# Optimization experiments

Hardware: AMD Instinct MI355X
Metric: run time of the kernel (lower is better)

Reference implementation:

```python
import jax, jax.numpy as jnp
import numpy as np

B, S, HID = 2, 2048, 2048
H, KV, D = 32, 4, 128
G = H // KV
EPS = 1e-6
SCALE = D ** -0.5
ROPE_THETA = 1000000.0


def setup_inputs() -> dict:
    key = jax.random.key(0)
    ks = jax.random.split(key, 6)
    hidden_states = jax.random.normal(ks[0], (B, S, HID), jnp.float32)
    # real RoPE tables (position_embeddings passed into forward)
    inv_freq = 1.0 / (ROPE_THETA ** (np.arange(0, D, 2, dtype=np.float32) / D))
    ang = np.arange(S, dtype=np.float32)[:, None] * inv_freq[None, :]  # [S, D/2]
    emb = np.concatenate([ang, ang], axis=-1)  # [S, D]
    cos = jnp.broadcast_to(jnp.asarray(np.cos(emb)), (B, S, D))
    sin = jnp.broadcast_to(jnp.asarray(np.sin(emb)), (B, S, D))
    sd = 0.02
    wq = jax.random.normal(ks[1], (H * D, HID), jnp.float32) * sd
    wk = jax.random.normal(ks[2], (KV * D, HID), jnp.float32) * sd
    wv = jax.random.normal(ks[3], (KV * D, HID), jnp.float32) * sd
    wo = jax.random.normal(ks[4], (HID, H * D), jnp.float32) * sd
    q_norm_w = jnp.ones((D,), jnp.float32)
    k_norm_w = jnp.ones((D,), jnp.float32)
    return {"hidden_states": hidden_states, "cos": cos, "sin": sin,
            "wq": wq, "wk": wk, "wv": wv, "wo": wo,
            "q_norm_w": q_norm_w, "k_norm_w": k_norm_w}


def _rms_norm(x, w):
    var = jnp.mean(jnp.square(x), axis=-1, keepdims=True)
    return x * jax.lax.rsqrt(var + EPS) * w


def _rotate_half(x):
    x1, x2 = jnp.split(x, 2, axis=-1)
    return jnp.concatenate([-x2, x1], axis=-1)


def _rope(x, cos, sin):
    # x: [B,S,N,D]; cos/sin: [B,S,1,D] (unsqueeze_dim=2)
    return x * cos + _rotate_half(x) * sin


def reference(hidden_states, cos, sin, wq, wk, wv, wo, q_norm_w, k_norm_w):
    x = hidden_states
    q = jnp.einsum('bsh,oh->bso', x, wq).reshape(B, S, H, D)
    k = jnp.einsum('bsh,oh->bso', x, wk).reshape(B, S, KV, D)
    v = jnp.einsum('bsh,oh->bso', x, wv).reshape(B, S, KV, D)
    q = _rms_norm(q, q_norm_w)
    k = _rms_norm(k, k_norm_w)
    c = cos[:, :, None, :]
    s = sin[:, :, None, :]
    q = _rope(q, c, s)
    k = _rope(k, c, s)
    # GQA causal attention, BSND layout
    qg = q.reshape(B, S, KV, G, D)
    scores = jnp.einsum('bqkgd,bskd->bkgqs', qg, k) * SCALE  # [B,KV,G,Sq,Sk]
    causal = jnp.tril(jnp.ones((S, S), bool))
    scores = jnp.where(causal, scores, jnp.finfo(scores.dtype).min)
    p = jax.nn.softmax(scores, axis=-1)
    out = jnp.einsum('bkgqs,bskd->bqkgd', p, v).reshape(B, S, H * D)
    return jnp.einsum('bso,ho->bsh', out, wo)
```

## Files before the change

kernel.cpp:

```cpp
#include <hip/hip_runtime.h>
#include <hip/hip_bf16.h>

typedef __attribute__((ext_vector_type(8))) short short8;
typedef __attribute__((ext_vector_type(4))) float f32x4;

#define DEVI static __device__ __forceinline__

constexpr int Bb = 2, Ss = 2048, Hh = 32, KVc = 4, Dc = 128;
constexpr float EPSc = 1e-6f;
constexpr float SCALEc = 0.08838834764831845f;

DEVI float bf2f(short s) {
  unsigned u = ((unsigned)(unsigned short)s) << 16;
  float f; __builtin_memcpy(&f, &u, 4); return f;
}
DEVI short f2bf(float f) {
  __hip_bfloat16 h = __float2bfloat16(f);
  unsigned short u; __builtin_memcpy(&u, &h, 2); return (short)u;
}

#define GLDS(gsrc, ldst) __builtin_amdgcn_global_load_lds( \
    (const __attribute__((address_space(1))) void*)(gsrc), \
    (__attribute__((address_space(3))) void*)(ldst), 16, 0, 0)

struct Cvt5 { const float* src[5]; short* dst[5]; };
__global__ void cvt_all(Cvt5 a) {
  constexpr int CUM[6] = {0, 2097152, 4194304, 4456448, 4718592, 6815744};
  const int stride = gridDim.x * blockDim.x;
  for (int i = blockIdx.x * blockDim.x + threadIdx.x; i < 6815744; i += stride) {
    int s = 0;
#pragma unroll
    for (int t = 1; t < 5; ++t) if (i >= CUM[t]) s = t;
    int j = i - CUM[s];
    float4 v = ((const float4*)a.src[s])[j];
    short4 o;
    o.x = f2bf(v.x); o.y = f2bf(v.y); o.z = f2bf(v.z); o.w = f2bf(v.w);
    ((short4*)a.dst[s])[j] = o;
  }
}

__launch_bounds__(512, 2)
__global__ void gemm8q(const short* __restrict__ A,
                       const short* __restrict__ Bp,
                       short* __restrict__ oq,
                       const float* __restrict__ cosb,
                       const float* __restrict__ sinb,
                       const float* __restrict__ qnw,
                       int K)
{
  __shared__ short lA[2][256 * 64];
  __shared__ short lB[2][256 * 64];

  const int tid = threadIdx.x, lane = tid & 63;
  const int wvi = tid >> 6;
  const int l15 = lane & 15, g = lane >> 4;
  const int wm = wvi >> 1, wn = wvi & 1;
  const int m0 = blockIdx.x * 256;
  const int n0 = blockIdx.y * 256;

  f32x4 acc[4][8] = {};

  auto stA = [&](int half, int slot, int kt) {
#pragma unroll
    for (int j = 0; j < 2; ++j) {
      int rr = j * 64 + (tid >> 3);
      int grow = ((rr >> 5) << 6) + half * 32 + (rr & 31);
      GLDS(A + (size_t)(m0 + grow) * K + kt * 64 + (((tid & 7) ^ (rr & 7)) << 3),
           &lA[slot][(half * 128 + j * 64) * 64 + tid * 8]);
    }
  };
  auto stB = [&](int half, int slot, int kt) {
#pragma unroll
    for (int j = 0; j < 2; ++j) {
      int rr = j * 64 + (tid >> 3);
      int gn = ((rr >> 6) << 7) + half * 64 + (rr & 63);
      GLDS(Bp + (size_t)(n0 + gn) * K + kt * 64 + (((tid & 7) ^ (rr & 7)) << 3),
           &lB[slot][(half * 128 + j * 64) * 64 + tid * 8]);
    }
  };

#define PH(SLOT, MH, NH, STG, GT) do {                                          \
    short8 afr[2][2], bfr[4][2];                                                \
    _Pragma("unroll")                                                           \
    for (int mi2 = 0; mi2 < 2; ++mi2) {                                         \
      int rp = (MH) * 128 + wm * 32 + mi2 * 16 + l15;                           \
      _Pragma("unroll")                                                         \
      for (int kk = 0; kk < 2; ++kk)                                            \
        afr[mi2][kk] = *(const short8*)(&lA[SLOT][rp * 64 +                     \
                         (((kk * 4 + g) ^ (rp & 7)) << 3)]);                    \
    }                                                                           \
    _Pragma("unroll")                                                           \
    for (int nj = 0; nj < 4; ++nj) {                                            \
      int rp = (NH) * 128 + wn * 64 + nj * 16 + l15;                            \
      _Pragma("unroll")                                                         \
      for (int kk = 0; kk < 2; ++kk)                                            \
        bfr[nj][kk] = *(const short8*)(&lB[SLOT][rp * 64 +                      \
                         (((kk * 4 + g) ^ (rp & 7)) << 3)]);                    \
    }                                                                           \
    STG;                                                                        \
    asm volatile("" ::: "memory");                                              \
    __builtin_amdgcn_s_barrier();                                               \
    __builtin_amdgcn_s_setprio(1);                                              \
    _Pragma("unroll")                                                           \
    for (int mi2 = 0; mi2 < 2; ++mi2)                                           \
      _Pragma("unroll")                                                         \
      for (int nj = 0; nj < 4; ++nj)                                            \
        _Pragma("unroll")                                                       \
        for (int kk = 0; kk < 2; ++kk)                                          \
          acc[(MH)*2 + mi2][(NH)*4 + nj] =                                      \
            __builtin_amdgcn_mfma_f32_16x16x32_bf16(afr[mi2][kk], bfr[nj][kk],  \
                acc[(MH)*2 + mi2][(NH)*4 + nj], 0, 0, 0);                       \
    __builtin_amdgcn_s_setprio(0);                                              \
    GT;                                                                         \
    asm volatile("" ::: "memory");                                              \
    __builtin_amdgcn_s_barrier();                                               \
  } while (0)

  const int nit = K >> 7;

  stA(0, 0, 0); stB(0, 0, 0); stA(1, 0, 0); stB(1, 0, 0);
  stA(0, 1, 1); stB(0, 1, 1);
  asm volatile("s_waitcnt vmcnt(4)" ::: "memory");
  __builtin_amdgcn_s_barrier();

  for (int it = 0; it < nit; ++it) {
    const int kt1 = 2 * it + 1;
    const int k2 = 2 * it + 2, k3 = 2 * it + 3;
    const bool pre = (it + 1 < nit);
    PH(0, 0, 0, { stA(1, 1, kt1); }, {});
    PH(0, 0, 1, { stB(1, 1, kt1); }, {});
    PH(0, 1, 0, { if (pre) stA(0, 0, k2); }, {});
    PH(0, 1, 1, { if (pre) stB(0, 0, k2); },
               { if (pre) asm volatile("s_waitcnt vmcnt(4)" ::: "memory");
                 else     asm volatile("s_waitcnt vmcnt(0)" ::: "memory"); });
    PH(1, 0, 0, { if (pre) stA(1, 0, k2); }, {});
    PH(1, 0, 1, { if (pre) stB(1, 0, k2); }, {});
    PH(1, 1, 0, { if (pre) stA(0, 1, k3); }, {});
    PH(1, 1, 1, { if (pre) stB(0, 1, k3); },
               { if (pre) asm volatile("s_waitcnt vmcnt(4)" ::: "memory"); });
  }
#undef PH

  float w8[8];
#pragma unroll
  for (int ni = 0; ni < 8; ++ni) w8[ni] = qnw[ni * 16 + l15];
#pragma unroll
  for (int mi = 0; mi < 4; ++mi)
#pragma unroll
    for (int r = 0; r < 4; ++r) {
      int m = m0 + wm * 64 + mi * 16 + g * 4 + r;
      int b = m >> 11, s = m & 2047;
      float xv[8];
      float ssq = 0.f;
#pragma unroll
      for (int ni = 0; ni < 8; ++ni) { xv[ni] = acc[mi][ni][r]; ssq += xv[ni] * xv[ni]; }
      ssq += __shfl_xor(ssq, 1);
      ssq += __shfl_xor(ssq, 2);
      ssq += __shfl_xor(ssq, 4);
      ssq += __shfl_xor(ssq, 8);
      float inv = rsqrtf(ssq * (1.0f / 128.0f) + EPSc);
      float xn[8];
#pragma unroll
      for (int ni = 0; ni < 8; ++ni) xn[ni] = xv[ni] * inv * w8[ni];
      const float* cpr = cosb + ((size_t)b * Ss + s) * Dc;
      const float* spr = sinb + ((size_t)b * Ss + s) * Dc;
#pragma unroll
      for (int ni = 0; ni < 8; ++ni) {
        int d = ni * 16 + l15;
        float c = cpr[d], sn = spr[d];
        float rot = (ni < 4) ? -xn[ni + 4] : xn[ni - 4];
        float o = xn[ni] * c + rot * sn;
        oq[(size_t)m * 4096 + n0 + wn * 128 + d] = f2bf(o * SCALEc);
      }
    }
}

template<int MODE>
__launch_bounds__(256, 4)
__global__ void gemm2(const short* __restrict__ A,
                      const short* __restrict__ B1,
                      const short* __restrict__ B2,
                      short* __restrict__ ok,
                      short* __restrict__ ov,
                      float* __restrict__ of,
                      const float* __restrict__ cosb,
                      const float* __restrict__ sinb,
                      const float* __restrict__ knw,
                      int K)
{
  __shared__ short lA[2][128 * 32];
  __shared__ short lB[2][128 * 32];
  const int tid = threadIdx.x;
  const int lane = tid & 63;
  const int wvi = tid >> 6;
  const int l15 = lane & 15, g = lane >> 4;
  const int m0 = blockIdx.x * 128;
  const int nt = blockIdx.y;
  const short* Bp; int n0, region;
  if (MODE == 0) {
    if (nt < 4) { Bp = B1; n0 = nt * 128;       region = 1; }
    else        { Bp = B2; n0 = (nt - 4) * 128; region = 2; }
  } else { Bp = B1; n0 = nt * 128; region = 3; }

  const int wrow = wvi * 32;
  const int srow = tid >> 2, schunk = tid & 3;

  f32x4 acc[2][8] = {};

  auto STAGE = [&](int ks, int bufi) {
    const int k0 = ks * 32;
#pragma unroll
    for (int c = 0; c < 2; ++c) {
      int row = c * 64 + srow;
      int gc = schunk ^ ((row >> 1) & 3);
      GLDS(A  + (size_t)(m0 + row) * K + k0 + gc * 8, &lA[bufi][(c * 256 + tid) * 8]);
      GLDS(Bp + (size_t)(n0 + row) * K + k0 + gc * 8, &lB[bufi][(c * 256 + tid) * 8]);
    }
  };

  const int nks = K >> 5;
  STAGE(0, 0);
  STAGE(1, 1);

  for (int ks = 0; ks < nks; ++ks) {
    const int cb = ks & 1;
    if (ks + 1 < nks) asm volatile("s_waitcnt vmcnt(4)" ::: "memory");
    else              asm volatile("s_waitcnt vmcnt(0)" ::: "memory");
    __builtin_amdgcn_s_barrier();
    asm volatile("" ::: "memory");

    short8 afr[2], bfr[8];
#pragma unroll
    for (int i = 0; i < 2; ++i) {
      int ra = wrow + i * 16 + l15;
      afr[i] = *(const short8*)(&lA[cb][0] + ra * 32 + ((g ^ ((ra >> 1) & 3)) * 8));
    }
#pragma unroll
    for (int i = 0; i < 8; ++i) {
      int rb = i * 16 + l15;
      bfr[i] = *(const short8*)(&lB[cb][0] + rb * 32 + ((g ^ ((rb >> 1) & 3)) * 8));
    }
#pragma unroll
    for (int mi = 0; mi < 2; ++mi)
#pragma unroll
      for (int ni = 0; ni < 8; ++ni)
        acc[mi][ni] = __builtin_amdgcn_mfma_f32_16x16x32_bf16(afr[mi], bfr[ni], acc[mi][ni], 0, 0, 0);

    asm volatile("" ::: "memory");
    __builtin_amdgcn_s_barrier();
    if (ks + 2 < nks) STAGE(ks + 2, cb);
  }

  if (MODE == 1) {
#pragma unroll
    for (int mi = 0; mi < 2; ++mi)
#pragma unroll
      for (int r = 0; r < 4; ++r) {
        int m = m0 + wrow + mi * 16 + g * 4 + r;
#pragma unroll
        for (int ni = 0; ni < 8; ++ni)
          of[(size_t)m * 2048 + n0 + ni * 16 + l15] = acc[mi][ni][r];
      }
  } else if (region == 2) {
#pragma unroll
    for (int mi = 0; mi < 2; ++mi)
#pragma unroll
      for (int r = 0; r < 4; ++r) {
        int m = m0 + wrow + mi * 16 + g * 4 + r;
        int b = m >> 11, s = m & 2047;
#pragma unroll
        for (int ni = 0; ni < 8; ++ni) {
          int n = n0 + ni * 16 + l15;
          int kvi = n >> 7, d = n & 127;
          ov[(((size_t)b * KVc + kvi) * 128 + d) * Ss + s] = f2bf(acc[mi][ni][r]);
        }
      }
  } else {
    float w8[8];
#pragma unroll
    for (int ni = 0; ni < 8; ++ni) w8[ni] = knw[ni * 16 + l15];
#pragma unroll
    for (int mi = 0; mi < 2; ++mi)
#pragma unroll
      for (int r = 0; r < 4; ++r) {
        int m = m0 + wrow + mi * 16 + g * 4 + r;
        int b = m >> 11, s = m & 2047;
        float xv[8];
        float ssq = 0.f;
#pragma unroll
        for (int ni = 0; ni < 8; ++ni) { xv[ni] = acc[mi][ni][r]; ssq += xv[ni] * xv[ni]; }
        ssq += __shfl_xor(ssq, 1);
        ssq += __shfl_xor(ssq, 2);
        ssq += __shfl_xor(ssq, 4);
        ssq += __shfl_xor(ssq, 8);
        float inv = rsqrtf(ssq * (1.0f / 128.0f) + EPSc);
        float xn[8];
#pragma unroll
        for (int ni = 0; ni < 8; ++ni) xn[ni] = xv[ni] * inv * w8[ni];
        const float* cpr = cosb + ((size_t)b * Ss + s) * Dc;
        const float* spr = sinb + ((size_t)b * Ss + s) * Dc;
#pragma unroll
        for (int ni = 0; ni < 8; ++ni) {
          int dl = ni * 16 + l15;
          float c = cpr[dl], sn = spr[dl];
          float rot = (ni < 4) ? -xn[ni + 4] : xn[ni - 4];
          float o = xn[ni] * c + rot * sn;
          int n = n0 + dl;
          int kvi = n >> 7, d = n & 127;
          ok[(((size_t)b * KVc + kvi) * Ss + s) * 128 + d] = f2bf(o);
        }
      }
  }
}

__launch_bounds__(256, 2)
__global__ void attn_fwd(const short* __restrict__ qb,
                         const short* __restrict__ kbuf,
                         const short* __restrict__ vtbuf,
                         short* __restrict__ ob)
{
  __shared__ short lK[2][64 * 128];
  __shared__ short lV[2][128 * 64];
  __shared__ short lP[4][32 * 32];
  const int tid = threadIdx.x, lane = tid & 63, wvi = tid >> 6;
  const int l15 = lane & 15, g = lane >> 4;
  const int pi = blockIdx.x, h = blockIdx.y, b = blockIdx.z;
  const int kv = h >> 3;
  const short* kp = kbuf  + ((size_t)b * KVc + kv) * Ss * 128;
  const short* vp = vtbuf + ((size_t)b * KVc + kv) * 128 * Ss;
  const int krow = tid >> 4, kch = tid & 15;
  const int vrow = tid >> 3, vch = tid & 7;

  for (int which = 0; which < 2; ++which) {
    const int qt = which ? (15 - pi) : pi;
    const int qwb = qt * 128 + wvi * 32;
    const int nkt = 2 * qt + 2;

    short8 qf[2][4];
#pragma unroll
    for (int qs = 0; qs < 2; ++qs)
#pragma unroll
      for (int dc = 0; dc < 4; ++dc)
        qf[qs][dc] = *(const short8*)(qb + (size_t)(b * Ss + qwb + qs * 16 + l15) * 4096
                                         + h * 128 + dc * 32 + g * 8);

    f32x4 oacc[2][8] = {};
    float mrun[2] = { -__builtin_inff(), -__builtin_inff() };
    float lrun[2] = { 0.f, 0.f };

    auto STAGE = [&](int kt, int bufi) {
      const int kb0 = kt * 64;
#pragma unroll
      for (int c = 0; c < 4; ++c) {
        int r = c * 16 + krow;
        int gc = kch ^ (r & 7);
        GLDS(kp + (size_t)(kb0 + r) * 128 + gc * 8, &lK[bufi][(c * 256 + tid) * 8]);
      }
#pragma unroll
      for (int c = 0; c < 4; ++c) {
        int r = c * 32 + vrow;
        int gc = vch ^ (r & 7);
        GLDS(vp + (size_t)r * Ss + kb0 + gc * 8, &lV[bufi][(c * 256 + tid) * 8]);
      }
    };

    STAGE(0, 0);
    STAGE(1, 1);

    for (int kt = 0; kt < nkt; ++kt) {
      const int cb = kt & 1;
      if (kt + 1 < nkt) asm volatile("s_waitcnt vmcnt(8)" ::: "memory");
      else              asm volatile("s_waitcnt vmcnt(0)" ::: "memory");
      __builtin_amdgcn_s_barrier();
      asm volatile("" ::: "memory");

#pragma unroll
      for (int half = 0; half < 2; ++half) {
        const int kb0 = kt * 64 + half * 32;
        if (kb0 <= qwb + 31) {
          short8 kf[2][4];
#pragma unroll
          for (int ks = 0; ks < 2; ++ks)
#pragma unroll
            for (int dc = 0; dc < 4; ++dc) {
              int row = half * 32 + ks * 16 + l15;
              kf[ks][dc] = *(const short8*)(&lK[cb][0] + row * 128 + (((dc * 4 + g) ^ (row & 7)) * 8));
            }
          f32x4 st[2][2] = {};
          __builtin_amdgcn_s_setprio(1);
#pragma unroll
          for (int qs = 0; qs < 2; ++qs)
#pragma unroll
            for (int ks = 0; ks < 2; ++ks)
#pragma unroll
              for (int dc = 0; dc < 4; ++dc)
                st[qs][ks] = __builtin_amdgcn_mfma_f32_16x16x32_bf16(kf[ks][dc], qf[qs][dc], st[qs][ks], 0, 0, 0);
          __builtin_amdgcn_s_setprio(0);

          const bool need_mask = (kb0 + 31 > qwb);
#pragma unroll
          for (int qs = 0; qs < 2; ++qs) {
            const int qg = qwb + qs * 16 + l15;
            float p[8];
            float tmax = -__builtin_inff();
#pragma unroll
            for (int ks = 0; ks < 2; ++ks)
#pragma unroll
              for (int r = 0; r < 4; ++r) {
                float v = st[qs][ks][r];
                if (need_mask && (kb0 + ks * 16 + g * 4 + r > qg)) v = -__builtin_inff();
                p[ks * 4 + r] = v;
                tmax = fmaxf(tmax, v);
              }
            tmax = fmaxf(tmax, __shfl_xor(tmax, 16));
            tmax = fmaxf(tmax, __shfl_xor(tmax, 32));
            float m_use = mrun[qs];
            if (__any(tmax > m_use + 8.0f)) {
              float mnew = fmaxf(m_use, tmax);
              float scl = __expf(m_use - mnew);
              lrun[qs] *= scl;
              mrun[qs] = mnew;
#pragma unroll
              for (int r = 0; r < 4; ++r) {
                float sc = __shfl(scl, g * 4 + r);
#pragma unroll
                for (int dt = 0; dt < 8; ++dt)
                  oacc[qs][dt][r] *= sc;
              }
              m_use = mnew;
            }
            float rsum = 0.f;
#pragma unroll
            for (int j = 0; j < 8; ++j) { p[j] = __expf(p[j] - m_use); rsum += p[j]; }
            rsum += __shfl_xor(rsum, 16);
            rsum += __shfl_xor(rsum, 32);
            lrun[qs] += rsum;
            {
              int row = qs * 16 + l15;
              int sw = (row >> 1) & 3;
              short* pr = lP[wvi] + row * 32;
#pragma unroll
              for (int ks = 0; ks < 2; ++ks) {
                int idx = (((2 * ks + (g >> 1)) ^ sw) * 8) + (g & 1) * 4;
                short4 pw;
                pw.x = f2bf(p[ks * 4 + 0]);
                pw.y = f2bf(p[ks * 4 + 1]);
                pw.z = f2bf(p[ks * 4 + 2]);
                pw.w = f2bf(p[ks * 4 + 3]);
                *(short4*)(pr + idx) = pw;
              }
            }
          }
          asm volatile("" ::: "memory");
          short8 vf[8];
#pragma unroll
          for (int dt = 0; dt < 8; ++dt) {
            int row = dt * 16 + l15;
            vf[dt] = *(const short8*)(&lV[cb][0] + row * 64 + (((half * 4 + g) ^ (row & 7)) * 8));
          }
          __builtin_amdgcn_s_setprio(1);
#pragma unroll
          for (int qs = 0; qs < 2; ++qs) {
            int row = qs * 16 + l15;
            short8 pf = *(const short8*)(lP[wvi] + row * 32 + ((g ^ ((row >> 1) & 3)) * 8));
#pragma unroll
            for (int dt = 0; dt < 8; ++dt)
              oacc[qs][dt] = __builtin_amdgcn_mfma_f32_16x16x32_bf16(pf, vf[dt], oacc[qs][dt], 0, 0, 0);
          }
          __builtin_amdgcn_s_setprio(0);
          asm volatile("" ::: "memory");
        }
      }

      asm volatile("" ::: "memory");
      __builtin_amdgcn_s_barrier();
      if (kt + 2 < nkt) STAGE(kt + 2, cb);
    }

#pragma unroll
    for (int qs = 0; qs < 2; ++qs)
#pragma unroll
      for (int r = 0; r < 4; ++r) {
        float inv = 1.0f / __shfl(lrun[qs], g * 4 + r);
        int qrow = qwb + qs * 16 + g * 4 + r;
        short* op = ob + (size_t)(b * Ss + qrow) * 4096 + h * 128;
#pragma unroll
        for (int dt = 0; dt < 8; ++dt)
          op[dt * 16 + l15] = f2bf(oacc[qs][dt][r] * inv);
      }
  }
}

extern "C" void kernel_launch(void* const* d_in, const int* in_sizes, int n_in,
                              void* d_out, int out_size, void* d_ws, size_t ws_size,
                              hipStream_t stream) {
  const float* x    = (const float*)d_in[0];
  const float* cosb = (const float*)d_in[1];
  const float* sinb = (const float*)d_in[2];
  const float* wq   = (const float*)d_in[3];
  const float* wk   = (const float*)d_in[4];
  const float* wv   = (const float*)d_in[5];
  const float* wo   = (const float*)d_in[6];
  const float* qw   = (const float*)d_in[7];
  const float* kw   = (const float*)d_in[8];

  size_t off = 0;
  auto alloc = [&](size_t bytes) {
    char* p = (char*)d_ws + off;
    off += (bytes + 255) & ~(size_t)255;
    return p;
  };
  short* x_bf  = (short*)alloc((size_t)8388608 * 2);
  short* wq_bf = (short*)alloc((size_t)8388608 * 2);
  short* wk_bf = (short*)alloc((size_t)1048576 * 2);
  short* wv_bf = (short*)alloc((size_t)1048576 * 2);
  short* wo_bf = (short*)alloc((size_t)8388608 * 2);
  short* q_bf  = (short*)alloc((size_t)16777216 * 2);
  short* k_bf  = (short*)alloc((size_t)2097152 * 2);
  short* v_bf  = (short*)alloc((size_t)2097152 * 2);
  short* ao_bf = (short*)alloc((size_t)16777216 * 2);

  Cvt5 ca;
  ca.src[0] = x;    ca.dst[0] = x_bf;
  ca.src[1] = wq;   ca.dst[1] = wq_bf;
  ca.src[2] = wk;   ca.dst[2] = wk_bf;
  ca.src[3] = wv;   ca.dst[3] = wv_bf;
  ca.src[4] = wo;   ca.dst[4] = wo_bf;
  cvt_all<<<2048, 256, 0, stream>>>(ca);

  gemm8q<<<dim3(16, 16), 512, 0, stream>>>(x_bf, wq_bf, q_bf, cosb, sinb, qw, 2048);
  gemm2<0><<<dim3(32, 8), 256, 0, stream>>>(x_bf, wk_bf, wv_bf, k_bf, v_bf, nullptr,
                                            cosb, sinb, kw, 2048);
  attn_fwd<<<dim3(8, 32, 2), 256, 0, stream>>>(q_bf, k_bf, v_bf, ao_bf);
  gemm2<1><<<dim3(32, 16), 256, 0, stream>>>(ao_bf, wo_bf, nullptr, nullptr, nullptr,
                                             (float*)d_out, nullptr, nullptr, nullptr, 4096);
}
```

Baseline: 346.4 us.

## Drop LDS K/V staging in attention; per-wave direct global loads with 512-thread blocks

```diff
diff --git a/kernel.cpp b/kernel.cpp
--- a/kernel.cpp
+++ b/kernel.cpp
@@ -9,6 +9,8 @@
 constexpr int Bb = 2, Ss = 2048, Hh = 32, KVc = 4, Dc = 128;
 constexpr float EPSc = 1e-6f;
 constexpr float SCALEc = 0.08838834764831845f;
+constexpr float LOG2Ec = 1.4426950408889634f;
+constexpr float SCALE2c = SCALEc * LOG2Ec;
 
 DEVI float bf2f(short s) {
   unsigned u = ((unsigned)(unsigned short)s) << 16;
@@ -170,7 +172,7 @@
         float c = cpr[d], sn = spr[d];
         float rot = (ni < 4) ? -xn[ni + 4] : xn[ni - 4];
         float o = xn[ni] * c + rot * sn;
-        oq[(size_t)m * 4096 + n0 + wn * 128 + d] = f2bf(o * SCALEc);
+        oq[(size_t)m * 4096 + n0 + wn * 128 + d] = f2bf(o * SCALE2c);
       }
     }
 }
@@ -313,182 +315,139 @@
   }
 }
 
-__launch_bounds__(256, 2)
+__launch_bounds__(512, 4)
 __global__ void attn_fwd(const short* __restrict__ qb,
                          const short* __restrict__ kbuf,
                          const short* __restrict__ vtbuf,
                          short* __restrict__ ob)
 {
-  __shared__ short lK[2][64 * 128];
-  __shared__ short lV[2][128 * 64];
-  __shared__ short lP[4][32 * 32];
+  __shared__ short lP[8][32 * 32];
   const int tid = threadIdx.x, lane = tid & 63, wvi = tid >> 6;
   const int l15 = lane & 15, g = lane >> 4;
   const int pi = blockIdx.x, h = blockIdx.y, b = blockIdx.z;
+  const int sub = wvi & 3;
+  const int qt = (wvi < 4) ? pi : (15 - pi);
+  const int qwb = qt * 128 + sub * 32;
   const int kv = h >> 3;
   const short* kp = kbuf  + ((size_t)b * KVc + kv) * Ss * 128;
   const short* vp = vtbuf + ((size_t)b * KVc + kv) * 128 * Ss;
-  const int krow = tid >> 4, kch = tid & 15;
-  const int vrow = tid >> 3, vch = tid & 7;
-
-  for (int which = 0; which < 2; ++which) {
-    const int qt = which ? (15 - pi) : pi;
-    const int qwb = qt * 128 + wvi * 32;
-    const int nkt = 2 * qt + 2;
-
-    short8 qf[2][4];
-#pragma unroll
-    for (int qs = 0; qs < 2; ++qs)
+
+  short8 qf[2][4];
+#pragma unroll
+  for (int qs = 0; qs < 2; ++qs)
+#pragma unroll
+    for (int dc = 0; dc < 4; ++dc)
+      qf[qs][dc] = *(const short8*)(qb + (size_t)(b * Ss + qwb + qs * 16 + l15) * 4096
+                                       + h * 128 + dc * 32 + g * 8);
+
+  f32x4 oacc[2][8] = {};
+  float mrun[2] = { -__builtin_inff(), -__builtin_inff() };
+  float lrun[2] = { 0.f, 0.f };
+
+  const int nkt = 4 * qt + sub + 1;
+
+  for (int kt = 0; kt < nkt; ++kt) {
+    const int kb0 = kt * 32;
+    f32x4 st[2][2] = {};
+#pragma unroll
+    for (int ks = 0; ks < 2; ++ks) {
+      short8 kf[4];
 #pragma unroll
       for (int dc = 0; dc < 4; ++dc)
-        qf[qs][dc] = *(const short8*)(qb + (size_t)(b * Ss + qwb + qs * 16 + l15) * 4096
-                                         + h * 128 + dc * 32 + g * 8);
-
-    f32x4 oacc[2][8] = {};
-    float mrun[2] = { -__builtin_inff(), -__builtin_inff() };
-    float lrun[2] = { 0.f, 0.f };
-
-    auto STAGE = [&](int kt, int bufi) {
-      const int kb0 = kt * 64;
-#pragma unroll
-      for (int c = 0; c < 4; ++c) {
-        int r = c * 16 + krow;
-        int gc = kch ^ (r & 7);
-        GLDS(kp + (size_t)(kb0 + r) * 128 + gc * 8, &lK[bufi][(c * 256 + tid) * 8]);
-      }
-#pragma unroll
-      for (int c = 0; c < 4; ++c) {
-        int r = c * 32 + vrow;
-        int gc = vch ^ (r & 7);
-        GLDS(vp + (size_t)r * Ss + kb0 + gc * 8, &lV[bufi][(c * 256 + tid) * 8]);
-      }
-    };
-
-    STAGE(0, 0);
-    STAGE(1, 1);
-
-    for (int kt = 0; kt < nkt; ++kt) {
-      const int cb = kt & 1;
-      if (kt + 1 < nkt) asm volatile("s_waitcnt vmcnt(8)" ::: "memory");
-      else              asm volatile("s_waitcnt vmcnt(0)" ::: "memory");
-      __builtin_amdgcn_s_barrier();
-      asm volatile("" ::: "memory");
-
-#pragma unroll
-      for (int half = 0; half < 2; ++half) {
-        const int kb0 = kt * 64 + half * 32;
-        if (kb0 <= qwb + 31) {
-          short8 kf[2][4];
-#pragma unroll
-          for (int ks = 0; ks < 2; ++ks)
-#pragma unroll
-            for (int dc = 0; dc < 4; ++dc) {
-              int row = half * 32 + ks * 16 + l15;
-              kf[ks][dc] = *(const short8*)(&lK[cb][0] + row * 128 + (((dc * 4 + g) ^ (row & 7)) * 8));
-            }
-          f32x4 st[2][2] = {};
-          __builtin_amdgcn_s_setprio(1);
-#pragma unroll
-          for (int qs = 0; qs < 2; ++qs)
-#pragma unroll
-            for (int ks = 0; ks < 2; ++ks)
-#pragma unroll
-              for (int dc = 0; dc < 4; ++dc)
-                st[qs][ks] = __builtin_amdgcn_mfma_f32_16x16x32_bf16(kf[ks][dc], qf[qs][dc], st[qs][ks], 0, 0, 0);
-          __builtin_amdgcn_s_setprio(0);
-
-          const bool need_mask = (kb0 + 31 > qwb);
-#pragma unroll
-          for (int qs = 0; qs < 2; ++qs) {
-            const int qg = qwb + qs * 16 + l15;
-            float p[8];
-            float tmax = -__builtin_inff();
-#pragma unroll
-            for (int ks = 0; ks < 2; ++ks)
-#pragma unroll
-              for (int r = 0; r < 4; ++r) {
-                float v = st[qs][ks][r];
-                if (need_mask && (kb0 + ks * 16 + g * 4 + r > qg)) v = -__builtin_inff();
-                p[ks * 4 + r] = v;
-                tmax = fmaxf(tmax, v);
-              }
-            tmax = fmaxf(tmax, __shfl_xor(tmax, 16));
-            tmax = fmaxf(tmax, __shfl_xor(tmax, 32));
-            float m_use = mrun[qs];
-            if (__any(tmax > m_use + 8.0f)) {
-              float mnew = fmaxf(m_use, tmax);
-              float scl = __expf(m_use - mnew);
-              lrun[qs] *= scl;
-              mrun[qs] = mnew;
-#pragma unroll
-              for (int r = 0; r < 4; ++r) {
-                float sc = __shfl(scl, g * 4 + r);
-#pragma unroll
-                for (int dt = 0; dt < 8; ++dt)
-                  oacc[qs][dt][r] *= sc;
-              }
-              m_use = mnew;
-            }
-            float rsum = 0.f;
-#pragma unroll
-            for (int j = 0; j < 8; ++j) { p[j] = __expf(p[j] - m_use); rsum += p[j]; }
-            rsum += __shfl_xor(rsum, 16);
-            rsum += __shfl_xor(rsum, 32);
-            lrun[qs] += rsum;
-            {
-              int row = qs * 16 + l15;
-              int sw = (row >> 1) & 3;
-              short* pr = lP[wvi] + row * 32;
-#pragma unroll
-              for (int ks = 0; ks < 2; ++ks) {
-                int idx = (((2 * ks + (g >> 1)) ^ sw) * 8) + (g & 1) * 4;
-                short4 pw;
-                pw.x = f2bf(p[ks * 4 + 0]);
-                pw.y = f2bf(p[ks * 4 + 1]);
-                pw.z = f2bf(p[ks * 4 + 2]);
-                pw.w = f2bf(p[ks * 4 + 3]);
-                *(short4*)(pr + idx) = pw;
-              }
-            }
-          }
-          asm volatile("" ::: "memory");
-          short8 vf[8];
-#pragma unroll
-          for (int dt = 0; dt < 8; ++dt) {
-            int row = dt * 16 + l15;
-            vf[dt] = *(const short8*)(&lV[cb][0] + row * 64 + (((half * 4 + g) ^ (row & 7)) * 8));
-          }
-          __builtin_amdgcn_s_setprio(1);
-#pragma unroll
-          for (int qs = 0; qs < 2; ++qs) {
-            int row = qs * 16 + l15;
-            short8 pf = *(const short8*)(lP[wvi] + row * 32 + ((g ^ ((row >> 1) & 3)) * 8));
-#pragma unroll
-            for (int dt = 0; dt < 8; ++dt)
-              oacc[qs][dt] = __builtin_amdgcn_mfma_f32_16x16x32_bf16(pf, vf[dt], oacc[qs][dt], 0, 0, 0);
-          }
-          __builtin_amdgcn_s_setprio(0);
-          asm volatile("" ::: "memory");
+        kf[dc] = *(const short8*)(kp + (size_t)(kb0 + ks * 16 + l15) * 128 + dc * 32 + g * 8);
+      __builtin_amdgcn_s_setprio(1);
+#pragma unroll
+      for (int qs = 0; qs < 2; ++qs)
+#pragma unroll
+        for (int dc = 0; dc < 4; ++dc)
+          st[qs][ks] = __builtin_amdgcn_mfma_f32_16x16x32_bf16(kf[dc], qf[qs][dc], st[qs][ks], 0, 0, 0);
+      __builtin_amdgcn_s_setprio(0);
+    }
+
+    const bool need_mask = (kt == nkt - 1);
+#pragma unroll
+    for (int qs = 0; qs < 2; ++qs) {
+      const int qg = qwb + qs * 16 + l15;
+      float p[8];
+      float tmax = -__builtin_inff();
+#pragma unroll
+      for (int ks = 0; ks < 2; ++ks)
+#pragma unroll
+        for (int r = 0; r < 4; ++r) {
+          float v = st[qs][ks][r];
+          if (need_mask && (kb0 + ks * 16 + g * 4 + r > qg)) v = -__builtin_inff();
+          p[ks * 4 + r] = v;
+          tmax = fmaxf(tmax, v);
         }
-      }
-
-      asm volatile("" ::: "memory");
-      __builtin_amdgcn_s_barrier();
-      if (kt + 2 < nkt) STAGE(kt + 2, cb);
-    }
-
-#pragma unroll
-    for (int qs = 0; qs < 2; ++qs)
-#pragma unroll
-      for (int r = 0; r < 4; ++r) {
-        float inv = 1.0f / __shfl(lrun[qs], g * 4 + r);
-        int qrow = qwb + qs * 16 + g * 4 + r;
-        short* op = ob + (size_t)(b * Ss + qrow) * 4096 + h * 128;
-#pragma unroll
-        for (int dt = 0; dt < 8; ++dt)
-          op[dt * 16 + l15] = f2bf(oacc[qs][dt][r] * inv);
-      }
+      tmax = fmaxf(tmax, __shfl_xor(tmax, 16));
+      tmax = fmaxf(tmax, __shfl_xor(tmax, 32));
+      float m_use = mrun[qs];
+      if (__any(tmax > m_use + 11.0f)) {
+        float mnew = fmaxf(m_use, tmax);
+        float scl = exp2f(m_use - mnew);
+        lrun[qs] *= scl;
+        mrun[qs] = mnew;
+#pragma unroll
+        for (int r = 0; r < 4; ++r) {
+          float sc = __shfl(scl, g * 4 + r);
+#pragma unroll
+          for (int dt = 0; dt < 8; ++dt)
+            oacc[qs][dt][r] *= sc;
+        }
+        m_use = mnew;
+      }
+      float rsum = 0.f;
+#pragma unroll
+      for (int j = 0; j < 8; ++j) { p[j] = exp2f(p[j] - m_use); rsum += p[j]; }
+      rsum += __shfl_xor(rsum, 16);
+      rsum += __shfl_xor(rsum, 32);
+      lrun[qs] += rsum;
+      {
+        int row = qs * 16 + l15;
+        int sw = (row >> 1) & 3;
+        short* pr = lP[wvi] + row * 32;
+#pragma unroll
+        for (int ks = 0; ks < 2; ++ks) {
+          int idx = (((2 * ks + (g >> 1)) ^ sw) * 8) + (g & 1) * 4;
+          short4 pw;
+          pw.x = f2bf(p[ks * 4 + 0]);
+          pw.y = f2bf(p[ks * 4 + 1]);
+          pw.z = f2bf(p[ks * 4 + 2]);
+          pw.w = f2bf(p[ks * 4 + 3]);
+          *(short4*)(pr + idx) = pw;
+        }
+      }
+    }
+    asm volatile("" ::: "memory");
+
+    short8 vf[8];
+#pragma unroll
+    for (int dt = 0; dt < 8; ++dt)
+      vf[dt] = *(const short8*)(vp + (size_t)(dt * 16 + l15) * Ss + kb0 + g * 8);
+    __builtin_amdgcn_s_setprio(1);
+#pragma unroll
+    for (int qs = 0; qs < 2; ++qs) {
+      int row = qs * 16 + l15;
+      short8 pf = *(const short8*)(lP[wvi] + row * 32 + ((g ^ ((row >> 1) & 3)) * 8));
+#pragma unroll
+      for (int dt = 0; dt < 8; ++dt)
+        oacc[qs][dt] = __builtin_amdgcn_mfma_f32_16x16x32_bf16(pf, vf[dt], oacc[qs][dt], 0, 0, 0);
+    }
+    __builtin_amdgcn_s_setprio(0);
+    asm volatile("" ::: "memory");
   }
+
+#pragma unroll
+  for (int qs = 0; qs < 2; ++qs)
+#pragma unroll
+    for (int r = 0; r < 4; ++r) {
+      float inv = 1.0f / __shfl(lrun[qs], g * 4 + r);
+      int qrow = qwb + qs * 16 + g * 4 + r;
+      short* op = ob + (size_t)(b * Ss + qrow) * 4096 + h * 128;
+#pragma unroll
+      for (int dt = 0; dt < 8; ++dt)
+        op[dt * 16 + l15] = f2bf(oacc[qs][dt][r] * inv);
+    }
 }
 
 extern "C" void kernel_launch(void* const* d_in, const int* in_sizes, int n_in,
@@ -531,7 +490,7 @@
   gemm8q<<<dim3(16, 16), 512, 0, stream>>>(x_bf, wq_bf, q_bf, cosb, sinb, qw, 2048);
   gemm2<0><<<dim3(32, 8), 256, 0, stream>>>(x_bf, wk_bf, wv_bf, k_bf, v_bf, nullptr,
                                             cosb, sinb, kw, 2048);
-  attn_fwd<<<dim3(8, 32, 2), 256, 0, stream>>>(q_bf, k_bf, v_bf, ao_bf);
+  attn_fwd<<<dim3(8, 32, 2), 512, 0, stream>>>(q_bf, k_bf, v_bf, ao_bf);
   gemm2<1><<<dim3(32, 16), 256, 0, stream>>>(ao_bf, wo_bf, nullptr, nullptr, nullptr,
                                              (float*)d_out, nullptr, nullptr, nullptr, 4096);
 }
```

After: 724.8 us. 2.09x slower.
